# Kernel tuning notes

Measured on AMD Instinct MI355X. Metric: run time of the kernel, lower is better.

## Reference

```python
import jax, jax.numpy as jnp
import numpy as np

N_NODES = 100000


def _gcn_conv(x, row, col, ew, W, b, n):
    # PyG GCNConv: add self-loops (weight 1), symmetric normalization,
    # linear transform, scatter-add aggregation at target, then bias.
    loop = jnp.arange(n, dtype=row.dtype)
    r = jnp.concatenate([row, loop])
    c = jnp.concatenate([col, loop])
    w = jnp.concatenate([ew, jnp.ones((n,), ew.dtype)])
    deg = jax.ops.segment_sum(w, c, num_segments=n)
    dinv = jnp.where(deg > 0, jax.lax.rsqrt(deg), 0.0)
    nrm = dinv[r] * w * dinv[c]                 # [E+N]
    h = x @ W                                    # [N, out]
    msg = h[r] * nrm[:, None]                    # gather + scale
    return jax.ops.segment_sum(msg, c, num_segments=n) + b


def setup_inputs() -> dict:
    key = jax.random.key(0)
    ks = jax.random.split(key, 16)
    n, e, f, s = N_NODES, 1600000, 8, 64
    return {
        "x": jax.random.normal(ks[0], (n, f), jnp.float32),
        "edge_index": jax.random.randint(ks[1], (2, e), 0, n, jnp.int32),
        "edge_weight": jax.random.uniform(ks[2], (e,), jnp.float32),
        "s_values": jax.random.normal(ks[3], (s,), jnp.float32),
        "s_fc1_w": jax.random.normal(ks[4], (s, s // 2), jnp.float32) * 0.1,
        "s_fc1_b": jax.random.normal(ks[5], (s // 2,), jnp.float32) * 0.1,
        "s_fc2_w": jax.random.normal(ks[6], (s // 2, 1), jnp.float32) * 0.1,
        "s_fc2_b": jax.random.normal(ks[7], (1,), jnp.float32) * 0.1,
        "conv1_w": jax.random.normal(ks[8], (f + 1, 32), jnp.float32) * 0.3,
        "conv1_b": jax.random.normal(ks[9], (32,), jnp.float32) * 0.1,
        "conv2_w": jax.random.normal(ks[10], (32, 16), jnp.float32) * 0.2,
        "conv2_b": jax.random.normal(ks[11], (16,), jnp.float32) * 0.1,
        "fc1_w": jax.random.normal(ks[12], (16, 1), jnp.float32) * 0.25,
        "fc1_b": jax.random.normal(ks[13], (1,), jnp.float32) * 0.1,
    }


def reference(x, edge_index, edge_weight, s_values,
              s_fc1_w, s_fc1_b, s_fc2_w, s_fc2_b,
              conv1_w, conv1_b, conv2_w, conv2_b, fc1_w, fc1_b):
    n = x.shape[0]
    row, col = edge_index[0], edge_index[1]
    # s-value encoder: two small linears, ReLU between
    s_enc = jax.nn.relu(s_values @ s_fc1_w + s_fc1_b) @ s_fc2_w + s_fc2_b  # [1]
    xs = jnp.concatenate([x, jnp.broadcast_to(s_enc[None, :], (n, 1))], axis=1)
    h1 = _gcn_conv(xs, row, col, edge_weight, conv1_w, conv1_b, n)
    h1 = jax.nn.leaky_relu(h1, 0.01)
    # dropout is identity in eval mode; norm=False skips GraphNorm
    h2 = _gcn_conv(h1, row, col, edge_weight, conv2_w, conv2_b, n)
    h2 = jax.nn.leaky_relu(h2, 0.01)
    return h2 @ fc1_w + fc1_b  # [N, 1]
```

## Files before the change

### kernel.cpp

```cpp
#include <hip/hip_runtime.h>
#include <hip/hip_fp16.h>


#define NBLKA  256
#define BSH    7
#define BNODES 128
#define MAXBK  784

__device__ inline unsigned enc_w(float w) {
    return ((unsigned)__half_as_ushort(__float2half_rn(w)) & 0x7FFFu) << 17;
}
__device__ inline float dec_w(unsigned e) {
    return __half2float(__ushort_as_half((unsigned short)((e >> 17) & 0x7FFFu)));
}

__global__ void k_hist(const int* __restrict__ ei, int* __restrict__ hist,
                       int E, int EPB, int NBK,
                       const float* __restrict__ x, __half* __restrict__ xh, int n,
                       const float* __restrict__ sv, const float* __restrict__ w1,
                       const float* __restrict__ b1, const float* __restrict__ w2,
                       const float* __restrict__ b2, float* __restrict__ senc) {
    if (blockIdx.x >= NBLKA) {
        if (blockIdx.x == gridDim.x - 1) {
            __shared__ float hid[32];
            int j = threadIdx.x;
            if (j < 32) {
                float acc = b1[j];
                #pragma unroll 8
                for (int k = 0; k < 64; ++k) acc += sv[k] * w1[k * 32 + j];
                hid[j] = acc > 0.f ? acc : 0.f;
            }
            __syncthreads();
            if (j == 0) {
                float acc = b2[0];
                #pragma unroll 8
                for (int k = 0; k < 32; ++k) acc += hid[k] * w2[k];
                senc[0] = acc;
            }
            return;
        }
        int i = (blockIdx.x - NBLKA) * blockDim.x + threadIdx.x;
        if (i >= n) return;
        const float4* xi = reinterpret_cast<const float4*>(x + (size_t)i * 8);
        float4 u = xi[0], v = xi[1];
        __half2 h0 = __floats2half2_rn(u.x, u.y);
        __half2 h1 = __floats2half2_rn(u.z, u.w);
        __half2 h2 = __floats2half2_rn(v.x, v.y);
        __half2 h3 = __floats2half2_rn(v.z, v.w);
        uint4 w;
        w.x = *reinterpret_cast<unsigned*>(&h0);
        w.y = *reinterpret_cast<unsigned*>(&h1);
        w.z = *reinterpret_cast<unsigned*>(&h2);
        w.w = *reinterpret_cast<unsigned*>(&h3);
        reinterpret_cast<uint4*>(xh + (size_t)i * 8)[0] = w;
        return;
    }
    __shared__ int lh[MAXBK];
    for (int k = threadIdx.x; k < NBK; k += blockDim.x) lh[k] = 0;
    __syncthreads();
    int b = blockIdx.x;
    int e0 = b * EPB, e1 = min(E, e0 + EPB);
    for (int e = e0 + threadIdx.x; e < e1; e += blockDim.x)
        atomicAdd(&lh[ei[E + e] >> BSH], 1);
    __syncthreads();
    for (int k = threadIdx.x; k < NBK; k += blockDim.x)
        hist[(size_t)k * NBLKA + b] = lh[k];
}

__global__ void k_scan1(int* __restrict__ data, int* __restrict__ bsum, int nflat) {
    __shared__ int s[512];
    int i = blockIdx.x * 512 + threadIdx.x;
    int v = (i < nflat) ? data[i] : 0;
    s[threadIdx.x] = v;
    __syncthreads();
    for (int off = 1; off < 512; off <<= 1) {
        int tv = (threadIdx.x >= off) ? s[threadIdx.x - off] : 0;
        __syncthreads();
        if (threadIdx.x >= off) s[threadIdx.x] += tv;
        __syncthreads();
    }
    if (i < nflat) data[i] = s[threadIdx.x] - v;
    if (threadIdx.x == 511) bsum[blockIdx.x] = s[511];
}

__global__ void k_scan2(int* __restrict__ bsum, int nb) {
    __shared__ int s[512];
    __shared__ int carry;
    if (threadIdx.x == 0) carry = 0;
    __syncthreads();
    for (int base = 0; base < nb; base += 512) {
        int idx = base + threadIdx.x;
        int v = (idx < nb) ? bsum[idx] : 0;
        s[threadIdx.x] = v;
        __syncthreads();
        for (int off = 1; off < 512; off <<= 1) {
            int tv = (threadIdx.x >= off) ? s[threadIdx.x - off] : 0;
            __syncthreads();
            if (threadIdx.x >= off) s[threadIdx.x] += tv;
            __syncthreads();
        }
        if (idx < nb) bsum[idx] = s[threadIdx.x] - v + carry;
        __syncthreads();
        if (threadIdx.x == 0) carry += s[511];
        __syncthreads();
    }
}

__global__ void k_scatter(const int* __restrict__ ei, const float* __restrict__ ew,
                          const int* __restrict__ scanned, const int* __restrict__ bsum,
                          int2* __restrict__ ebuf, int E, int EPB, int NBK) {
    __shared__ int lbase[MAXBK];
    int b = blockIdx.x;
    for (int k = threadIdx.x; k < NBK; k += blockDim.x) {
        int idx = k * NBLKA + b;
        lbase[k] = scanned[idx] + bsum[idx >> 9];
    }
    __syncthreads();
    int e0 = b * EPB, e1 = min(E, e0 + EPB);
    for (int e = e0 + threadIdx.x; e < e1; e += blockDim.x) {
        int c = ei[E + e];
        int r = ei[e];
        int k = c >> BSH;
        int pos = atomicAdd(&lbase[k], 1);
        ebuf[pos] = make_int2(r | ((c & (BNODES - 1)) << 25), __float_as_int(ew[e]));
    }
}

__global__ void k_sort(const int* __restrict__ scanned, const int* __restrict__ bsum,
                       const int2* __restrict__ ebuf,
                       int* __restrict__ row, float* __restrict__ dinv,
                       unsigned* __restrict__ csr4, int n, int E, int NBK) {
    __shared__ int lcnt[BNODES];
    __shared__ int lofs[BNODES];
    __shared__ float lw[BNODES];
    int k = blockIdx.x;
    if (threadIdx.x < BNODES) { lcnt[threadIdx.x] = 0; lw[threadIdx.x] = 1.0f; }
    __syncthreads();
    int idx0 = k * NBLKA;
    int bs = scanned[idx0] + bsum[idx0 >> 9];
    int be = E;
    if (k + 1 < NBK) {
        int idx1 = (k + 1) * NBLKA;
        be = scanned[idx1] + bsum[idx1 >> 9];
    }
    for (int s = bs + threadIdx.x; s < be; s += blockDim.x) {
        int2 ent = ebuf[s];
        int cl = ((unsigned)ent.x) >> 25;
        atomicAdd(&lcnt[cl], 1);
        atomicAdd(&lw[cl], __int_as_float(ent.y));
    }
    __syncthreads();
    int v = (threadIdx.x < BNODES) ? lcnt[threadIdx.x] : 0;
    if (threadIdx.x < BNODES) lofs[threadIdx.x] = v;
    __syncthreads();
    for (int off = 1; off < BNODES; off <<= 1) {
        int tv = 0;
        if (threadIdx.x < BNODES && threadIdx.x >= off) tv = lofs[threadIdx.x - off];
        __syncthreads();
        if (threadIdx.x < BNODES && threadIdx.x >= off) lofs[threadIdx.x] += tv;
        __syncthreads();
    }
    if (threadIdx.x < BNODES) {
        int excl = lofs[threadIdx.x] - v;
        lofs[threadIdx.x] = excl;
        int i = k * BNODES + threadIdx.x;
        if (i < n) {
            row[i] = bs + excl;
            dinv[i] = rsqrtf(lw[threadIdx.x]);
        }
    }
    if (k == NBK - 1 && threadIdx.x == 0) row[n] = E;
    __syncthreads();
    for (int s = bs + threadIdx.x; s < be; s += blockDim.x) {
        int2 ent = ebuf[s];
        int cl = ((unsigned)ent.x) >> 25;
        int pos = bs + atomicAdd(&lofs[cl], 1);
        csr4[pos] = enc_w(__int_as_float(ent.y)) | (unsigned)(ent.x & 0x1FFFF);
    }
}

__global__ void k_pass1(const int* __restrict__ row, unsigned* __restrict__ csr4,
                        const float* __restrict__ dinv, const __half* __restrict__ xh,
                        const float* __restrict__ senc,
                        const float* __restrict__ W1, const float* __restrict__ b1,
                        const float* __restrict__ W2, __half* __restrict__ th, int n) {
    __shared__ float sW1[288];
    __shared__ float sb1[32];
    __shared__ float sW2[32 * 17];
    for (int j = threadIdx.x; j < 288; j += blockDim.x) sW1[j] = W1[j];
    for (int j = threadIdx.x; j < 512; j += blockDim.x) sW2[(j >> 4) * 17 + (j & 15)] = W2[j];
    if (threadIdx.x < 32) sb1[threadIdx.x] = b1[threadIdx.x];
    __syncthreads();
    int g = blockIdx.x * blockDim.x + threadIdx.x;
    int i = g >> 3;
    int oct = g & 7;
    if (i >= n) return;
    float di = dinv[i];
    float a[8];
    float sw;
    if (oct == 0) {
        const uint4* xp = reinterpret_cast<const uint4*>(xh + (size_t)i * 8);
        uint4 w = xp[0];
        const __half2* hh = reinterpret_cast<const __half2*>(&w);
        #pragma unroll
        for (int q = 0; q < 4; ++q) {
            float2 f = __half22float2(hh[q]);
            a[2 * q] = di * f.x; a[2 * q + 1] = di * f.y;
        }
        sw = di;
    } else {
        #pragma unroll
        for (int q = 0; q < 8; ++q) a[q] = 0.f;
        sw = 0.f;
    }
    int s0 = row[i], s1 = row[i + 1];
    for (int s = s0 + oct; s < s1; s += 8) {
        unsigned ent = csr4[s];
        unsigned src = ent & 0x1FFFFu;
        float wpre = dec_w(ent) * dinv[src];
        csr4[s] = enc_w(wpre) | src;
        const uint4* xp = reinterpret_cast<const uint4*>(xh + (size_t)src * 8);
        uint4 w = xp[0];
        const __half2* hh = reinterpret_cast<const __half2*>(&w);
        #pragma unroll
        for (int q = 0; q < 4; ++q) {
            float2 f = __half22float2(hh[q]);
            a[2 * q] += wpre * f.x; a[2 * q + 1] += wpre * f.y;
        }
        sw += wpre;
    }
    #pragma unroll
    for (int m = 1; m <= 4; m <<= 1) {
        #pragma unroll
        for (int q = 0; q < 8; ++q) a[q] += __shfl_xor(a[q], m);
        sw += __shfl_xor(sw, m);
    }
    float a8 = di * sw * senc[0];
    float af[8];
    #pragma unroll
    for (int q = 0; q < 8; ++q) af[q] = di * a[q];
    float h[4];
    #pragma unroll
    for (int jj = 0; jj < 4; ++jj) {
        int j = oct * 4 + jj;
        float acc = sb1[j] + a8 * sW1[8 * 32 + j];
        #pragma unroll
        for (int f = 0; f < 8; ++f) acc += af[f] * sW1[f * 32 + j];
        h[jj] = acc > 0.f ? acc : 0.01f * acc;
    }
    float p[16];
    #pragma unroll
    for (int o = 0; o < 16; ++o) p[o] = 0.f;
    #pragma unroll
    for (int jj = 0; jj < 4; ++jj) {
        int j = oct * 4 + jj;
        #pragma unroll
        for (int o = 0; o < 16; ++o) p[o] += h[jj] * sW2[j * 17 + o];
    }
    #pragma unroll
    for (int m = 1; m <= 4; m <<= 1) {
        #pragma unroll
        for (int o = 0; o < 16; ++o) p[o] += __shfl_xor(p[o], m);
    }
    __half2 hv = __floats2half2_rn(p[oct * 2], p[oct * 2 + 1]);
    reinterpret_cast<unsigned*>(th + (size_t)i * 16)[oct] =
        *reinterpret_cast<unsigned*>(&hv);
}

__global__ void k_pass2(const int* __restrict__ row, const unsigned* __restrict__ csr4,
                        const float* __restrict__ dinv, const __half* __restrict__ th,
                        const float* __restrict__ b2, const float* __restrict__ fw,
                        const float* __restrict__ fb, float* __restrict__ out, int n) {
    __shared__ float sb2[16];
    __shared__ float sfw[16];
    if (threadIdx.x < 16) { sb2[threadIdx.x] = b2[threadIdx.x]; sfw[threadIdx.x] = fw[threadIdx.x]; }
    __syncthreads();
    int g = blockIdx.x * blockDim.x + threadIdx.x;
    int i = g >> 3;
    int oct = g & 7;
    if (i >= n) return;
    float di = dinv[i];
    float acc[16];
    if (oct == 0) {
        const uint4* tp = reinterpret_cast<const uint4*>(th + (size_t)i * 16);
        uint4 w0 = tp[0], w1 = tp[1];
        const __half2* hh0 = reinterpret_cast<const __half2*>(&w0);
        const __half2* hh1 = reinterpret_cast<const __half2*>(&w1);
        #pragma unroll
        for (int q = 0; q < 4; ++q) {
            float2 f0 = __half22float2(hh0[q]);
            float2 f1 = __half22float2(hh1[q]);
            acc[2 * q + 0] = di * f0.x; acc[2 * q + 1] = di * f0.y;
            acc[8 + 2 * q + 0] = di * f1.x; acc[8 + 2 * q + 1] = di * f1.y;
        }
    } else {
        #pragma unroll
        for (int q = 0; q < 16; ++q) acc[q] = 0.f;
    }
    int s0 = row[i], s1 = row[i + 1];
    for (int s = s0 + oct; s < s1; s += 8) {
        unsigned ent = csr4[s];
        float wpre = dec_w(ent);
        const uint4* tp = reinterpret_cast<const uint4*>(th + (size_t)(ent & 0x1FFFFu) * 16);
        uint4 w0 = tp[0], w1 = tp[1];
        const __half2* hh0 = reinterpret_cast<const __half2*>(&w0);
        const __half2* hh1 = reinterpret_cast<const __half2*>(&w1);
        #pragma unroll
        for (int q = 0; q < 4; ++q) {
            float2 f0 = __half22float2(hh0[q]);
            float2 f1 = __half22float2(hh1[q]);
            acc[2 * q + 0] += wpre * f0.x; acc[2 * q + 1] += wpre * f0.y;
            acc[8 + 2 * q + 0] += wpre * f1.x; acc[8 + 2 * q + 1] += wpre * f1.y;
        }
    }
    #pragma unroll
    for (int m = 1; m <= 4; m <<= 1) {
        #pragma unroll
        for (int q = 0; q < 16; ++q) acc[q] += __shfl_xor(acc[q], m);
    }
    if (oct) return;
    float o = fb[0];
    #pragma unroll
    for (int q = 0; q < 16; ++q) {
        float v = di * acc[q] + sb2[q];
        v = v > 0.f ? v : 0.01f * v;
        o += v * sfw[q];
    }
    out[i] = o;
}

extern "C" void kernel_launch(void* const* d_in, const int* in_sizes, int n_in,
                              void* d_out, int out_size, void* d_ws, size_t ws_size,
                              hipStream_t stream) {
    const float* x      = (const float*)d_in[0];
    const int*   ei     = (const int*)d_in[1];
    const float* ew     = (const float*)d_in[2];
    const float* sv     = (const float*)d_in[3];
    const float* sfc1w  = (const float*)d_in[4];
    const float* sfc1b  = (const float*)d_in[5];
    const float* sfc2w  = (const float*)d_in[6];
    const float* sfc2b  = (const float*)d_in[7];
    const float* conv1w = (const float*)d_in[8];
    const float* conv1b = (const float*)d_in[9];
    const float* conv2w = (const float*)d_in[10];
    const float* conv2b = (const float*)d_in[11];
    const float* fc1w   = (const float*)d_in[12];
    const float* fc1b   = (const float*)d_in[13];

    const int n = in_sizes[0] / 8;
    const int E = in_sizes[2];

    const int NBK   = (n + BNODES - 1) >> BSH;
    const int nflat = NBK * NBLKA;
    const int EPB   = (E + NBLKA - 1) / NBLKA;
    const int nb1   = (nflat + 511) / 512;
    const int gX    = (n + 1023) / 1024;

    size_t off = 0;
    auto alloc = [&](size_t words) { size_t o = off; off += (words + 3) & ~(size_t)3; return o; };
    float*    base = (float*)d_ws;
    float*    senc = base + alloc(4);
    float*    dinv = base + alloc(n);
    int*      rowp = (int*)(base + alloc(n + 1));
    int*      hist = (int*)(base + alloc(nflat));
    int*      bsum = (int*)(base + alloc(512));
    int2*     ebuf = (int2*)(base + alloc((size_t)2 * E));
    unsigned* csr4 = (unsigned*)(base + alloc(E));
    __half*   xh   = (__half*)(base + alloc((size_t)4 * n));
    __half*   th   = (__half*)(base + alloc((size_t)8 * n));

    const int BT = 256;
    const int g8 = ((size_t)8 * n + BT - 1) / BT;

    k_hist<<<NBLKA + gX + 1, 1024, 0, stream>>>(ei, hist, E, EPB, NBK,
                                                x, xh, n,
                                                sv, sfc1w, sfc1b, sfc2w, sfc2b, senc);
    k_scan1<<<nb1, 512, 0, stream>>>(hist, bsum, nflat);
    k_scan2<<<1, 512, 0, stream>>>(bsum, nb1);
    k_scatter<<<NBLKA, 1024, 0, stream>>>(ei, ew, hist, bsum, ebuf, E, EPB, NBK);
    k_sort<<<NBK, 512, 0, stream>>>(hist, bsum, ebuf, rowp, dinv, csr4, n, E, NBK);
    k_pass1<<<g8, BT, 0, stream>>>(rowp, csr4, dinv, xh, senc,
                                   conv1w, conv1b, conv2w, th, n);
    k_pass2<<<g8, BT, 0, stream>>>(rowp, csr4, dinv, th,
                                   conv2b, fc1w, fc1b, (float*)d_out, n);
}
```

Measured before the change: 99.41 us.

## Fuse block-sum scan into scatter/sort, prefetch CSR entries, enlarge pass blocks

Removes the single-block k_scan2 launch by having every k_scatter and k_sort block redundantly scan the block sums in shared memory. The pass1/pass2 edge loops are software-pipelined so the next CSR entry loads while the current gather is consumed. Pass kernels now launch with 1024-thread blocks, and pass2 reads bias/fc weights directly instead of staging them in shared memory. The redundant per-block scan adds a little work to each block, and this assumes nb1 ≤ 512 (here 784*256/512 = 392) and that pass1 has no 256-thread shared-memory assumption.

Result: no change. 101.0 us (+1.6%).

```diff
diff --git a/kernel.cpp b/kernel.cpp
--- a/kernel.cpp
+++ b/kernel.cpp
@@ -83,37 +83,34 @@
     if (threadIdx.x == 511) bsum[blockIdx.x] = s[511];
 }
 
-__global__ void k_scan2(int* __restrict__ bsum, int nb) {
-    __shared__ int s[512];
-    __shared__ int carry;
-    if (threadIdx.x == 0) carry = 0;
-    __syncthreads();
-    for (int base = 0; base < nb; base += 512) {
-        int idx = base + threadIdx.x;
-        int v = (idx < nb) ? bsum[idx] : 0;
-        s[threadIdx.x] = v;
-        __syncthreads();
-        for (int off = 1; off < 512; off <<= 1) {
-            int tv = (threadIdx.x >= off) ? s[threadIdx.x - off] : 0;
-            __syncthreads();
-            if (threadIdx.x >= off) s[threadIdx.x] += tv;
-            __syncthreads();
-        }
-        if (idx < nb) bsum[idx] = s[threadIdx.x] - v + carry;
-        __syncthreads();
-        if (threadIdx.x == 0) carry += s[511];
-        __syncthreads();
-    }
+__device__ inline void scan_bsum(const int* __restrict__ bsum, int* sbs, int nb) {
+    int v = 0;
+    if (threadIdx.x < 512) {
+        v = (threadIdx.x < nb) ? bsum[threadIdx.x] : 0;
+        sbs[threadIdx.x] = v;
+    }
+    __syncthreads();
+    for (int off = 1; off < 512; off <<= 1) {
+        int tv = 0;
+        if (threadIdx.x < 512 && threadIdx.x >= off) tv = sbs[threadIdx.x - off];
+        __syncthreads();
+        if (threadIdx.x < 512 && threadIdx.x >= off) sbs[threadIdx.x] += tv;
+        __syncthreads();
+    }
+    if (threadIdx.x < 512) sbs[threadIdx.x] -= v;
+    __syncthreads();
 }
 
 __global__ void k_scatter(const int* __restrict__ ei, const float* __restrict__ ew,
                           const int* __restrict__ scanned, const int* __restrict__ bsum,
-                          int2* __restrict__ ebuf, int E, int EPB, int NBK) {
+                          int2* __restrict__ ebuf, int E, int EPB, int NBK, int nb) {
+    __shared__ int sbs[512];
     __shared__ int lbase[MAXBK];
+    scan_bsum(bsum, sbs, nb);
     int b = blockIdx.x;
     for (int k = threadIdx.x; k < NBK; k += blockDim.x) {
         int idx = k * NBLKA + b;
-        lbase[k] = scanned[idx] + bsum[idx >> 9];
+        lbase[k] = scanned[idx] + sbs[idx >> 9];
     }
     __syncthreads();
     int e0 = b * EPB, e1 = min(E, e0 + EPB);
@@ -129,19 +126,21 @@
 __global__ void k_sort(const int* __restrict__ scanned, const int* __restrict__ bsum,
                        const int2* __restrict__ ebuf,
                        int* __restrict__ row, float* __restrict__ dinv,
-                       unsigned* __restrict__ csr4, int n, int E, int NBK) {
+                       unsigned* __restrict__ csr4, int n, int E, int NBK, int nb) {
+    __shared__ int sbs[512];
     __shared__ int lcnt[BNODES];
     __shared__ int lofs[BNODES];
     __shared__ float lw[BNODES];
+    scan_bsum(bsum, sbs, nb);
     int k = blockIdx.x;
     if (threadIdx.x < BNODES) { lcnt[threadIdx.x] = 0; lw[threadIdx.x] = 1.0f; }
     __syncthreads();
     int idx0 = k * NBLKA;
-    int bs = scanned[idx0] + bsum[idx0 >> 9];
+    int bs = scanned[idx0] + sbs[idx0 >> 9];
     int be = E;
     if (k + 1 < NBK) {
         int idx1 = (k + 1) * NBLKA;
-        be = scanned[idx1] + bsum[idx1 >> 9];
+        be = scanned[idx1] + sbs[idx1 >> 9];
     }
     for (int s = bs + threadIdx.x; s < be; s += blockDim.x) {
         int2 ent = ebuf[s];
@@ -214,13 +213,18 @@
         sw = 0.f;
     }
     int s0 = row[i], s1 = row[i + 1];
-    for (int s = s0 + oct; s < s1; s += 8) {
-        unsigned ent = csr4[s];
+    int s = s0 + oct;
+    bool have = s < s1;
+    unsigned ent = have ? csr4[s] : 0u;
+    while (have) {
         unsigned src = ent & 0x1FFFFu;
-        float wpre = dec_w(ent) * dinv[src];
+        uint4 w = reinterpret_cast<const uint4*>(xh + (size_t)src * 8)[0];
+        float dv = dinv[src];
+        int s2 = s + 8;
+        bool have2 = s2 < s1;
+        unsigned entn = have2 ? csr4[s2] : 0u;
+        float wpre = dec_w(ent) * dv;
         csr4[s] = enc_w(wpre) | src;
-        const uint4* xp = reinterpret_cast<const uint4*>(xh + (size_t)src * 8);
-        uint4 w = xp[0];
         const __half2* hh = reinterpret_cast<const __half2*>(&w);
         #pragma unroll
         for (int q = 0; q < 4; ++q) {
@@ -228,6 +232,7 @@
             a[2 * q] += wpre * f.x; a[2 * q + 1] += wpre * f.y;
         }
         sw += wpre;
+        ent = entn; s = s2; have = have2;
     }
     #pragma unroll
     for (int m = 1; m <= 4; m <<= 1) {
@@ -271,10 +276,6 @@
                         const float* __restrict__ dinv, const __half* __restrict__ th,
                         const float* __restrict__ b2, const float* __restrict__ fw,
                         const float* __restrict__ fb, float* __restrict__ out, int n) {
-    __shared__ float sb2[16];
-    __shared__ float sfw[16];
-    if (threadIdx.x < 16) { sb2[threadIdx.x] = b2[threadIdx.x]; sfw[threadIdx.x] = fw[threadIdx.x]; }
-    __syncthreads();
     int g = blockIdx.x * blockDim.x + threadIdx.x;
     int i = g >> 3;
     int oct = g & 7;
@@ -298,11 +299,17 @@
         for (int q = 0; q < 16; ++q) acc[q] = 0.f;
     }
     int s0 = row[i], s1 = row[i + 1];
-    for (int s = s0 + oct; s < s1; s += 8) {
-        unsigned ent = csr4[s];
+    int s = s0 + oct;
+    bool have = s < s1;
+    unsigned ent = have ? csr4[s] : 0u;
+    while (have) {
+        unsigned src = ent & 0x1FFFFu;
+        const uint4* tp = reinterpret_cast<const uint4*>(th + (size_t)src * 16);
+        uint4 w0 = tp[0], w1 = tp[1];
+        int s2 = s + 8;
+        bool have2 = s2 < s1;
+        unsigned entn = have2 ? csr4[s2] : 0u;
         float wpre = dec_w(ent);
-        const uint4* tp = reinterpret_cast<const uint4*>(th + (size_t)(ent & 0x1FFFFu) * 16);
-        uint4 w0 = tp[0], w1 = tp[1];
         const __half2* hh0 = reinterpret_cast<const __half2*>(&w0);
         const __half2* hh1 = reinterpret_cast<const __half2*>(&w1);
         #pragma unroll
@@ -312,6 +319,7 @@
             acc[2 * q + 0] += wpre * f0.x; acc[2 * q + 1] += wpre * f0.y;
             acc[8 + 2 * q + 0] += wpre * f1.x; acc[8 + 2 * q + 1] += wpre * f1.y;
         }
+        ent = entn; s = s2; have = have2;
     }
     #pragma unroll
     for (int m = 1; m <= 4; m <<= 1) {
@@ -322,9 +330,9 @@
     float o = fb[0];
     #pragma unroll
     for (int q = 0; q < 16; ++q) {
-        float v = di * acc[q] + sb2[q];
+        float v = di * acc[q] + b2[q];
         v = v > 0.f ? v : 0.01f * v;
-        o += v * sfw[q];
+        o += v * fw[q];
     }
     out[i] = o;
 }
@@ -369,18 +377,16 @@
     __half*   xh   = (__half*)(base + alloc((size_t)4 * n));
     __half*   th   = (__half*)(base + alloc((size_t)8 * n));
 
-    const int BT = 256;
-    const int g8 = ((size_t)8 * n + BT - 1) / BT;
+    const int g8 = ((size_t)8 * n + 1023) / 1024;
 
     k_hist<<<NBLKA + gX + 1, 1024, 0, stream>>>(ei, hist, E, EPB, NBK,
                                                 x, xh, n,
                                                 sv, sfc1w, sfc1b, sfc2w, sfc2b, senc);
     k_scan1<<<nb1, 512, 0, stream>>>(hist, bsum, nflat);
-    k_scan2<<<1, 512, 0, stream>>>(bsum, nb1);
-    k_scatter<<<NBLKA, 1024, 0, stream>>>(ei, ew, hist, bsum, ebuf, E, EPB, NBK);
-    k_sort<<<NBK, 512, 0, stream>>>(hist, bsum, ebuf, rowp, dinv, csr4, n, E, NBK);
-    k_pass1<<<g8, BT, 0, stream>>>(rowp, csr4, dinv, xh, senc,
-                                   conv1w, conv1b, conv2w, th, n);
-    k_pass2<<<g8, BT, 0, stream>>>(rowp, csr4, dinv, th,
-                                   conv2b, fc1w, fc1b, (float*)d_out, n);
-}
+    k_scatter<<<NBLKA, 1024, 0, stream>>>(ei, ew, hist, bsum, ebuf, E, EPB, NBK, nb1);
+    k_sort<<<NBK, 512, 0, stream>>>(hist, bsum, ebuf, rowp, dinv, csr4, n, E, NBK, nb1);
+    k_pass1<<<g8, 1024, 0, stream>>>(rowp, csr4, dinv, xh, senc,
+                                     conv1w, conv1b, conv2w, th, n);
+    k_pass2<<<g8, 1024, 0, stream>>>(rowp, csr4, dinv, th,
+                                     conv2b, fc1w, fc1b, (float*)d_out, n);
+}
```
